# Kernel tuning notes

Measured on AMD Instinct MI355X. Metric: run time of the kernel, lower is better.

The kernel has to match this reference:

```python
import jax, jax.numpy as jnp
import numpy as np

B, L, A, K = 2, 1024, 14, 30
NUM_RBF = 16
NPE = 16  # num_positional_embeddings
EF = 128  # edge_features
EDGE_IN = NPE + NUM_RBF * A * A  # 3152


def setup_inputs() -> dict:
    key = jax.random.key(0)
    ks = jax.random.split(key, 4)
    # coords scaled so pairwise distances span the RBF range [0, 20]
    X = jax.random.normal(ks[0], (B, L, A, 3), dtype=jnp.float32) * 3.0
    mask = jnp.ones((B, L), dtype=jnp.float32)
    residue_idx = jnp.tile(jnp.arange(L, dtype=jnp.int32)[None, :], (B, 1))
    chain_labels = jnp.zeros((B, L), dtype=jnp.int32)
    atom_mask = jax.random.randint(ks[1], (B, L, A), 0, 2).astype(jnp.float32)
    W_edge = jax.random.normal(ks[2], (EF, EDGE_IN), dtype=jnp.float32) * 0.02
    ln_gamma = jnp.ones((EF,), dtype=jnp.float32)
    ln_beta = jnp.zeros((EF,), dtype=jnp.float32)
    return {"X": X, "mask": mask, "residue_idx": residue_idx,
            "chain_labels": chain_labels, "atom_mask": atom_mask,
            "W_edge": W_edge, "ln_gamma": ln_gamma, "ln_beta": ln_beta}


def reference(X, mask, residue_idx, chain_labels, atom_mask, W_edge, ln_gamma, ln_beta):
    Bq, Lq = X.shape[0], X.shape[1]
    # ---- CA pairwise distances + masked top-k (smallest) ----
    X_ca = X[:, :, 1, :]
    m2 = mask[:, :, None] * mask[:, None, :]                    # [B,L,L]
    dX = X_ca[:, :, None, :] - X_ca[:, None, :, :]
    D = m2 * jnp.sqrt(jnp.sum(dX ** 2, -1) + 1e-6)
    D_max = jnp.max(D, -1, keepdims=True)
    D_adjust = D + 2.0 * (1.0 - m2) * D_max
    _, E_idx = jax.lax.top_k(-D_adjust, K)                      # smallest K -> [B,L,K]
    # ---- transformer positional encoding of relative index ----
    ii = jnp.arange(Lq, dtype=jnp.float32)[None, :, None]
    d = (E_idx.astype(jnp.float32) - ii)[..., None]             # [B,L,K,1]
    freq = jnp.exp(jnp.arange(0, NPE, 2, dtype=jnp.float32) * (-(np.log(10000.0) / NPE)))
    angles = d * freq                                           # [B,L,K,NPE/2]
    E_pos = jnp.concatenate([jnp.cos(angles), jnp.sin(angles)], -1)  # [B,L,K,NPE]
    # ---- impute CB, build 14-atom set ----
    N_, Ca, C_, O_ = X[:, :, 0, :], X[:, :, 1, :], X[:, :, 2, :], X[:, :, 3, :]
    b = Ca - N_
    c = C_ - Ca
    a = jnp.cross(b, c)
    Cb = -0.58273431 * a + 0.56802827 * b - 0.54067466 * c + Ca
    X2 = jnp.concatenate([jnp.stack([N_, Ca, C_, O_, Cb], -2), X[:, :, 5:, :]], -2)  # [B,L,14,3]
    am = 1.0 - atom_mask                                        # module passes 1 - atom_mask
    # ---- gather neighbor atoms, fused 14x14 atom-pair RBFs ----
    bidx = jnp.arange(Bq)[:, None, None]
    X2n = X2[bidx, E_idx]                                       # [B,L,K,14,3]
    amn = am[bidx, E_idx]                                       # [B,L,K,14]
    diff = X2[:, :, None, :, None, :] - X2n[:, :, :, None, :, :]
    Dab = jnp.sqrt(jnp.sum(diff ** 2, -1) + 1e-6)               # [B,L,K,14,14] (a of i, b of nbr)
    combo = am[:, :, None, :, None] * amn[:, :, :, None, :]     # [B,L,K,14,14]
    mu = jnp.linspace(0.0, 20.0, NUM_RBF)
    sigma = 20.0 / NUM_RBF
    rbf = jnp.exp(-(((Dab[..., None] - mu) / sigma) ** 2)) * combo[..., None]
    RBF_all = rbf.reshape(Bq, Lq, K, A * A * NUM_RBF)           # matches torch cat order (i,j,rbf)
    # ---- edge embedding + layernorm ----
    E = jnp.concatenate([E_pos, RBF_all], -1)                   # [B,L,K,EDGE_IN]
    E = E @ W_edge.T                                            # [B,L,K,EF]
    mean = jnp.mean(E, -1, keepdims=True)
    var = jnp.var(E, -1, keepdims=True)
    E = (E - mean) / jnp.sqrt(var + 1e-5) * ln_gamma + ln_beta
    return (E, E_idx)
```

## Files before the change

kernel.cpp:

```cpp
#include <hip/hip_runtime.h>
#include <hip/hip_bf16.h>
#include <stdint.h>

#define LQ 1024
#define BQ 2
#define AQ 14
#define KQ 30
#define EFQ 128
#define EDGE_IN 3152
#define KPAD 3200
#define NCHUNK 50
#define ROWS (BQ*LQ*KQ)
#define EIDX_OFF (ROWS*EFQ)

typedef __attribute__((ext_vector_type(8))) _Float16 half8;
typedef __attribute__((ext_vector_type(4))) float floatx4;
typedef unsigned long long ull;

static __device__ __forceinline__ uint32_t pkh(float a, float b) {
    auto h = __builtin_amdgcn_cvt_pkrtz(a, b);
    return __builtin_bit_cast(uint32_t, h);
}

__global__ __launch_bounds__(512) void topk_kernel(
    const float* __restrict__ X, const float* __restrict__ mask,
    float* __restrict__ out, int* __restrict__ idx_ws)
{
    __shared__ float xs[LQ], ys[LQ], zs[LQ], ms[LQ];

    const int t = threadIdx.x, w = t >> 6, lane = t & 63;
    const int row = blockIdx.x*8 + w;
    const int b = row >> 10, i = row & (LQ - 1);

    for (int j = t; j < LQ; j += 512) {
        size_t base = ((size_t)(b*LQ + j))*42 + 3;
        xs[j] = X[base+0]; ys[j] = X[base+1]; zs[j] = X[base+2];
        ms[j] = mask[b*LQ + j];
    }
    __syncthreads();

    const float mif = ms[i];
    const double cx = (double)xs[i], cy = (double)ys[i], cz = (double)zs[i];

    double Dk[16]; float mf[16];
    bool allone = (mif == 1.0f);
    #pragma unroll
    for (int s = 0; s < 16; ++s) {
        int j = s*64 + lane;
        double dx = __dsub_rn(cx, (double)xs[j]);
        double dy = __dsub_rn(cy, (double)ys[j]);
        double dz = __dsub_rn(cz, (double)zs[j]);
        mf[s] = ms[j];
        Dk[s] = __dadd_rn(__dadd_rn(__dmul_rn(dx,dx), __dmul_rn(dy,dy)),
                          __dmul_rn(dz,dz));
        allone = allone && (mf[s] == 1.0f);
    }

    if (!__all(allone ? 1 : 0)) {
        const double mi_d = (double)mif;
        double lm = 0.0;
        #pragma unroll
        for (int s = 0; s < 16; ++s) {
            double m2 = __dmul_rn(mi_d, (double)mf[s]);
            Dk[s] = __dmul_rn(m2, sqrt(__dadd_rn(Dk[s], 1e-6)));
            lm = fmax(lm, Dk[s]);
        }
        #pragma unroll
        for (int off = 32; off; off >>= 1) lm = fmax(lm, __shfl_xor(lm, off));
        #pragma unroll
        for (int s = 0; s < 16; ++s) {
            double m2 = __dmul_rn(mi_d, (double)mf[s]);
            Dk[s] = __dadd_rn(Dk[s],
                    __dmul_rn(__dmul_rn(2.0, __dsub_rn(1.0, m2)), lm));
        }
    }

    unsigned cons = 0;
    for (int k = 0; k < KQ; ++k) {
        ull bk = ~0ull; int bi = 1 << 30;
        #pragma unroll
        for (int s = 0; s < 16; ++s) {
            ull key = (ull)__double_as_longlong(Dk[s]);
            bool alive = !((cons >> s) & 1u);
            if (alive && key < bk) { bk = key; bi = s*64 + lane; }
        }
        #pragma unroll
        for (int off = 32; off; off >>= 1) {
            ull okk = __shfl_xor(bk, off);
            int oii = __shfl_xor(bi, off);
            if (okk < bk || (okk == bk && oii < bi)) { bk = okk; bi = oii; }
        }
        if ((bi & 63) == lane) cons |= (1u << (bi >> 6));
        if (lane == 0) {
            int rg = row*KQ + k;
            idx_ws[rg] = bi;
            out[EIDX_OFF + rg] = (float)bi;
        }
    }
}

__global__ __launch_bounds__(256) void wpad_kernel(
    const float* __restrict__ W, _Float16* __restrict__ wpad)
{
    int idx = blockIdx.x*256 + threadIdx.x;
    if (idx >= EFQ*KPAD) return;
    int n = idx / KPAD, f = idx - n*KPAD;
    float v = (f < EDGE_IN) ? W[(size_t)n*EDGE_IN + f] : 0.0f;
    wpad[idx] = (_Float16)v;
}

struct FusedSmem {
    alignas(16) float atoms[128*42];
    alignas(16) unsigned short Bl[128*64];
    alignas(16) float drow[64];
    int residg[128];
    unsigned int maskb[128];
    float gsh[EFQ], bsh[EFQ];
};

static __device__ __forceinline__ void gen8(
    const float* __restrict__ atomsA, const float* __restrict__ atomsB,
    unsigned maskA, unsigned maskB, float drowv,
    int f0, uint32_t* __restrict__ v)
{
    if (f0 >= 16) {
        int p = (f0 - 16) >> 4;
        if (p >= AQ*AQ) { v[0] = v[1] = v[2] = v[3] = 0u; return; }
        int rbase = (f0 - 16) & 15;
        int a  = (p * 74899) >> 20;
        int bp = p - a*14;
        bool czero = ((((maskA >> a) | (maskB >> bp)) & 1u) != 0u);
        const float* ca = atomsA + a*3;
        const float* na = atomsB + bp*3;
        float dx = ca[0]-na[0], dy = ca[1]-na[1], dz = ca[2]-na[2];
        float u = __builtin_amdgcn_sqrtf(dx*dx + dy*dy + dz*dz + 1e-6f) * 0.96089846f;
        float e[8];
        #pragma unroll
        for (int j = 0; j < 8; ++j) {
            float tt = __fmaf_rn(-(float)(rbase + j), 1.28119795f, u);
            e[j] = __builtin_amdgcn_exp2f(-(tt*tt));
        }
        #pragma unroll
        for (int k = 0; k < 4; ++k) v[k] = czero ? 0u : pkh(e[2*k], e[2*k+1]);
    } else {
        const float fr[8] = {1.0f, 0.31622776601683794f, 0.1f,
            0.031622776601683794f, 0.01f, 0.0031622776601683794f,
            0.001f, 0.00031622776601683794f};
        float e[8];
        if (f0 == 0) {
            #pragma unroll
            for (int j = 0; j < 8; ++j) e[j] = __cosf(drowv * fr[j]);
        } else {
            #pragma unroll
            for (int j = 0; j < 8; ++j) e[j] = __sinf(drowv * fr[j]);
        }
        #pragma unroll
        for (int k = 0; k < 4; ++k) v[k] = pkh(e[2*k], e[2*k+1]);
    }
}

__global__ __launch_bounds__(256) void fused_kernel(
    const float* __restrict__ X, const float* __restrict__ atom_mask,
    const _Float16* __restrict__ wpad, const float* __restrict__ gamma,
    const float* __restrict__ beta, const int* __restrict__ idx_ws,
    float* __restrict__ out)
{
    __shared__ FusedSmem sm;
    const int t = threadIdx.x;
    const int row0 = blockIdx.x * 64;
    const int b = row0 / (LQ*KQ);

    if (t < 64) {
        int rg = row0 + t;
        int rem = rg - b*(LQ*KQ);
        int i = rem / KQ;
        int j = idx_ws[rg];
        sm.residg[t]    = b*LQ + i;
        sm.residg[64+t] = b*LQ + j;
        sm.drow[t] = (float)j - (float)i;
    }
    if (t < EFQ) { sm.gsh[t] = gamma[t]; sm.bsh[t] = beta[t]; }
    __syncthreads();

    for (int u = t; u < 128*42; u += 256) {
        int s = u / 42; int e = u - s*42;
        sm.atoms[s*42 + e] = X[(size_t)sm.residg[s]*42 + e];
    }
    __syncthreads();

    if (t < 128) {
        float* at = &sm.atoms[t*42];
        float Nx=at[0],Ny=at[1],Nz=at[2], Cax=at[3],Cay=at[4],Caz=at[5],
              Cx=at[6],Cy=at[7],Cz=at[8];
        float bx=Cax-Nx, by=Cay-Ny, bz=Caz-Nz;
        float ex=Cx-Cax, ey=Cy-Cay, ez=Cz-Caz;
        float ax = by*ez - bz*ey, ay = bz*ex - bx*ez, az = bx*ey - by*ex;
        at[12] = -0.58273431f*ax + 0.56802827f*bx - 0.54067466f*ex + Cax;
        at[13] = -0.58273431f*ay + 0.56802827f*by - 0.54067466f*ey + Cay;
        at[14] = -0.58273431f*az + 0.56802827f*bz - 0.54067466f*ez + Caz;
        unsigned mb = 0;
        const float* amp = &atom_mask[(size_t)sm.residg[t]*AQ];
        #pragma unroll
        for (int a = 0; a < AQ; ++a) if (amp[a] > 0.5f) mb |= (1u << a);
        sm.maskb[t] = mb;
    }

    const int w = t >> 6, lane = t & 63, q = lane >> 4, l15 = lane & 15;
    const int m = w*16 + l15;

    int boff0[8], boff1[8];
    #pragma unroll
    for (int nt = 0; nt < 8; ++nt) {
        int n = nt*16 + l15;
        boff0[nt] = n*64 + ((q ^ (n&7))*8);
        boff1[nt] = n*64 + (((4+q) ^ (n&7))*8);
    }
    int stRegion[4]; const _Float16* stBase[4];
    #pragma unroll
    for (int i2 = 0; i2 < 4; ++i2) {
        int region = w*4 + i2;
        int n = region*8 + (lane >> 3);
        int kbsrc = (lane & 7) ^ (lane >> 3);
        stRegion[i2] = region;
        stBase[i2] = wpad + (size_t)n*KPAD + kbsrc*8;
    }
    auto stage = [&](int c) {
        #pragma unroll
        for (int i2 = 0; i2 < 4; ++i2) {
            const _Float16* g = stBase[i2] + c*64;
            __builtin_amdgcn_global_load_lds(
                (const __attribute__((address_space(1))) uint32_t*)g,
                (__attribute__((address_space(3))) uint32_t*)&sm.Bl[stRegion[i2]*512],
                16, 0, 0);
        }
    };

    floatx4 acc[8];
    #pragma unroll
    for (int nt = 0; nt < 8; ++nt) acc[nt] = (floatx4){0.f,0.f,0.f,0.f};

    __syncthreads();

    const float* atomsA = &sm.atoms[m*42];
    const float* atomsB = &sm.atoms[(64+m)*42];
    const unsigned maskA = sm.maskb[m], maskB = sm.maskb[64+m];
    const float drowv = sm.drow[m];

    union H8 { uint32_t u[4]; half8 h; };
    for (int c = 0; c < NCHUNK; ++c) {
        if (c) __syncthreads();
        stage(c);
        H8 va0, va1;
        gen8(atomsA, atomsB, maskA, maskB, drowv, c*64 + q*8,      va0.u);
        gen8(atomsA, atomsB, maskA, maskB, drowv, c*64 + 32 + q*8, va1.u);
        __syncthreads();
        #pragma unroll
        for (int nt = 0; nt < 8; ++nt) {
            half8 b0 = *reinterpret_cast<const half8*>(&sm.Bl[boff0[nt]]);
            half8 b1 = *reinterpret_cast<const half8*>(&sm.Bl[boff1[nt]]);
            acc[nt] = __builtin_amdgcn_mfma_f32_16x16x32_f16(va0.h, b0, acc[nt], 0, 0, 0);
            acc[nt] = __builtin_amdgcn_mfma_f32_16x16x32_f16(va1.h, b1, acc[nt], 0, 0, 0);
        }
    }

    #pragma unroll
    for (int v = 0; v < 4; ++v) {
        float s = 0.f, s2 = 0.f;
        #pragma unroll
        for (int nt = 0; nt < 8; ++nt) { float x = acc[nt][v]; s += x; s2 += x*x; }
        #pragma unroll
        for (int off = 1; off < 16; off <<= 1) {
            s  += __shfl_xor(s,  off);
            s2 += __shfl_xor(s2, off);
        }
        float mean = s * (1.0f/128.0f);
        float var  = s2 * (1.0f/128.0f) - mean*mean;
        float rstd = 1.0f / sqrtf(var + 1e-5f);
        int row_l = w*16 + q*4 + v;
        size_t obase = (size_t)(row0 + row_l)*EFQ;
        #pragma unroll
        for (int nt = 0; nt < 8; ++nt) {
            int col = nt*16 + l15;
            out[obase + col] = (acc[nt][v] - mean)*rstd*sm.gsh[col] + sm.bsh[col];
        }
    }
}

extern "C" void kernel_launch(void* const* d_in, const int* in_sizes, int n_in,
                              void* d_out, int out_size, void* d_ws, size_t ws_size,
                              hipStream_t stream)
{
    const float* X         = (const float*)d_in[0];
    const float* mask      = (const float*)d_in[1];
    const float* atom_mask = (const float*)d_in[4];
    const float* W         = (const float*)d_in[5];
    const float* gamma     = (const float*)d_in[6];
    const float* beta      = (const float*)d_in[7];
    float* out = (float*)d_out;

    int*       idx_ws = (int*)d_ws;
    _Float16*  wpad   = (_Float16*)((char*)d_ws + 262144);

    hipLaunchKernelGGL(wpad_kernel, dim3((EFQ*KPAD + 255)/256), dim3(256), 0, stream,
                       W, wpad);
    hipLaunchKernelGGL(topk_kernel, dim3(BQ*LQ/8), dim3(512), 0, stream,
                       X, mask, out, idx_ws);
    hipLaunchKernelGGL(fused_kernel, dim3(ROWS/64), dim3(256), 0, stream,
                       X, atom_mask, wpad, gamma, beta, idx_ws, out);
}
```

Before: 189.8 us.

## Merge weight padding into top-k launch, pack top-k keys, double fused M tile

Drops the separate weight-padding kernel by having the extra blocks of the top-k launch do the fp16 conversion. The top-k selection now packs each neighbor index into the low bits of its distance key, so each round is a plain 64-bit min tree and no separate index comparison is needed. The fused RBF+GEMM kernel moves to 512 threads and 128 rows per block, so each staged weight chunk is shared by twice as many rows. In exchange there are fewer blocks, more shared memory per block, and the key packing truncates the low 10 mantissa bits, which could change the order of near-tied distances.

New measurement: 176.2 us. 7.1% less time.

```diff
diff --git a/kernel.cpp b/kernel.cpp
--- a/kernel.cpp
+++ b/kernel.cpp
@@ -10,6 +10,7 @@
 #define EDGE_IN 3152
 #define KPAD 3200
 #define NCHUNK 50
+#define MTILE 128
 #define ROWS (BQ*LQ*KQ)
 #define EIDX_OFF (ROWS*EFQ)
 
@@ -21,14 +22,29 @@
     auto h = __builtin_amdgcn_cvt_pkrtz(a, b);
     return __builtin_bit_cast(uint32_t, h);
 }
+static __device__ __forceinline__ ull umin64(ull a, ull b) { return a < b ? a : b; }
 
 __global__ __launch_bounds__(512) void topk_kernel(
     const float* __restrict__ X, const float* __restrict__ mask,
-    float* __restrict__ out, int* __restrict__ idx_ws)
+    const float* __restrict__ W, float* __restrict__ out,
+    int* __restrict__ idx_ws, _Float16* __restrict__ wpad)
 {
     __shared__ float xs[LQ], ys[LQ], zs[LQ], ms[LQ];
-
-    const int t = threadIdx.x, w = t >> 6, lane = t & 63;
+    const int t = threadIdx.x;
+
+    if (blockIdx.x >= 256) {
+        int base = (blockIdx.x - 256)*8192 + t;
+        #pragma unroll
+        for (int r = 0; r < 16; ++r) {
+            int idx = base + r*512;
+            int n = idx / KPAD, f = idx - n*KPAD;
+            float v = (f < EDGE_IN) ? W[(size_t)n*EDGE_IN + f] : 0.0f;
+            wpad[idx] = (_Float16)v;
+        }
+        return;
+    }
+
+    const int w = t >> 6, lane = t & 63;
     const int row = blockIdx.x*8 + w;
     const int b = row >> 10, i = row & (LQ - 1);
 
@@ -75,46 +91,43 @@
         }
     }
 
-    unsigned cons = 0;
+    ull key[16];
+    #pragma unroll
+    for (int s = 0; s < 16; ++s)
+        key[s] = (((ull)__double_as_longlong(Dk[s])) & ~1023ull)
+               | (unsigned)(s*64 + lane);
+
     for (int k = 0; k < KQ; ++k) {
-        ull bk = ~0ull; int bi = 1 << 30;
-        #pragma unroll
-        for (int s = 0; s < 16; ++s) {
-            ull key = (ull)__double_as_longlong(Dk[s]);
-            bool alive = !((cons >> s) & 1u);
-            if (alive && key < bk) { bk = key; bi = s*64 + lane; }
-        }
-        #pragma unroll
-        for (int off = 32; off; off >>= 1) {
-            ull okk = __shfl_xor(bk, off);
-            int oii = __shfl_xor(bi, off);
-            if (okk < bk || (okk == bk && oii < bi)) { bk = okk; bi = oii; }
-        }
-        if ((bi & 63) == lane) cons |= (1u << (bi >> 6));
+        ull a0 = umin64(key[0],  key[1]),  a1 = umin64(key[2],  key[3]);
+        ull a2 = umin64(key[4],  key[5]),  a3 = umin64(key[6],  key[7]);
+        ull a4 = umin64(key[8],  key[9]),  a5 = umin64(key[10], key[11]);
+        ull a6 = umin64(key[12], key[13]), a7 = umin64(key[14], key[15]);
+        ull b0 = umin64(a0, a1), b1 = umin64(a2, a3);
+        ull b2 = umin64(a4, a5), b3 = umin64(a6, a7);
+        ull bk = umin64(umin64(b0, b1), umin64(b2, b3));
+        #pragma unroll
+        for (int off = 32; off; off >>= 1)
+            bk = umin64(bk, (ull)__shfl_xor(bk, off));
+        int j = (int)(bk & 1023ull);
         if (lane == 0) {
             int rg = row*KQ + k;
-            idx_ws[rg] = bi;
-            out[EIDX_OFF + rg] = (float)bi;
-        }
-    }
-}
-
-__global__ __launch_bounds__(256) void wpad_kernel(
-    const float* __restrict__ W, _Float16* __restrict__ wpad)
-{
-    int idx = blockIdx.x*256 + threadIdx.x;
-    if (idx >= EFQ*KPAD) return;
-    int n = idx / KPAD, f = idx - n*KPAD;
-    float v = (f < EDGE_IN) ? W[(size_t)n*EDGE_IN + f] : 0.0f;
-    wpad[idx] = (_Float16)v;
+            idx_ws[rg] = j;
+            out[EIDX_OFF + rg] = (float)j;
+        }
+        bool mine = ((j & 63) == lane);
+        int s_win = j >> 6;
+        #pragma unroll
+        for (int s = 0; s < 16; ++s)
+            key[s] = (mine && s == s_win) ? ~0ull : key[s];
+    }
 }
 
 struct FusedSmem {
-    alignas(16) float atoms[128*42];
+    alignas(16) float atoms[256*42];
     alignas(16) unsigned short Bl[128*64];
-    alignas(16) float drow[64];
-    int residg[128];
-    unsigned int maskb[128];
+    alignas(16) float drow[MTILE];
+    int residg[256];
+    unsigned int maskb[256];
     float gsh[EFQ], bsh[EFQ];
 };
 
@@ -159,7 +172,7 @@
     }
 }
 
-__global__ __launch_bounds__(256) void fused_kernel(
+__global__ __launch_bounds__(512) void fused_kernel(
     const float* __restrict__ X, const float* __restrict__ atom_mask,
     const _Float16* __restrict__ wpad, const float* __restrict__ gamma,
     const float* __restrict__ beta, const int* __restrict__ idx_ws,
@@ -167,28 +180,28 @@
 {
     __shared__ FusedSmem sm;
     const int t = threadIdx.x;
-    const int row0 = blockIdx.x * 64;
+    const int row0 = blockIdx.x * MTILE;
     const int b = row0 / (LQ*KQ);
 
-    if (t < 64) {
+    if (t < MTILE) {
         int rg = row0 + t;
         int rem = rg - b*(LQ*KQ);
         int i = rem / KQ;
         int j = idx_ws[rg];
-        sm.residg[t]    = b*LQ + i;
-        sm.residg[64+t] = b*LQ + j;
+        sm.residg[t]       = b*LQ + i;
+        sm.residg[MTILE+t] = b*LQ + j;
         sm.drow[t] = (float)j - (float)i;
     }
     if (t < EFQ) { sm.gsh[t] = gamma[t]; sm.bsh[t] = beta[t]; }
     __syncthreads();
 
-    for (int u = t; u < 128*42; u += 256) {
+    for (int u = t; u < 256*42; u += 512) {
         int s = u / 42; int e = u - s*42;
         sm.atoms[s*42 + e] = X[(size_t)sm.residg[s]*42 + e];
     }
     __syncthreads();
 
-    if (t < 128) {
+    if (t < 256) {
         float* at = &sm.atoms[t*42];
         float Nx=at[0],Ny=at[1],Nz=at[2], Cax=at[3],Cay=at[4],Caz=at[5],
               Cx=at[6],Cy=at[7],Cz=at[8];
@@ -215,10 +228,10 @@
         boff0[nt] = n*64 + ((q ^ (n&7))*8);
         boff1[nt] = n*64 + (((4+q) ^ (n&7))*8);
     }
-    int stRegion[4]; const _Float16* stBase[4];
-    #pragma unroll
-    for (int i2 = 0; i2 < 4; ++i2) {
-        int region = w*4 + i2;
+    int stRegion[2]; const _Float16* stBase[2];
+    #pragma unroll
+    for (int i2 = 0; i2 < 2; ++i2) {
+        int region = w*2 + i2;
         int n = region*8 + (lane >> 3);
         int kbsrc = (lane & 7) ^ (lane >> 3);
         stRegion[i2] = region;
@@ -226,7 +239,7 @@
     }
     auto stage = [&](int c) {
         #pragma unroll
-        for (int i2 = 0; i2 < 4; ++i2) {
+        for (int i2 = 0; i2 < 2; ++i2) {
             const _Float16* g = stBase[i2] + c*64;
             __builtin_amdgcn_global_load_lds(
                 (const __attribute__((address_space(1))) uint32_t*)g,
@@ -242,8 +255,8 @@
     __syncthreads();
 
     const float* atomsA = &sm.atoms[m*42];
-    const float* atomsB = &sm.atoms[(64+m)*42];
-    const unsigned maskA = sm.maskb[m], maskB = sm.maskb[64+m];
+    const float* atomsB = &sm.atoms[(MTILE+m)*42];
+    const unsigned maskA = sm.maskb[m], maskB = sm.maskb[MTILE+m];
     const float drowv = sm.drow[m];
 
     union H8 { uint32_t u[4]; half8 h; };
@@ -301,10 +314,8 @@
     int*       idx_ws = (int*)d_ws;
     _Float16*  wpad   = (_Float16*)((char*)d_ws + 262144);
 
-    hipLaunchKernelGGL(wpad_kernel, dim3((EFQ*KPAD + 255)/256), dim3(256), 0, stream,
-                       W, wpad);
-    hipLaunchKernelGGL(topk_kernel, dim3(BQ*LQ/8), dim3(512), 0, stream,
-                       X, mask, out, idx_ws);
-    hipLaunchKernelGGL(fused_kernel, dim3(ROWS/64), dim3(256), 0, stream,
+    hipLaunchKernelGGL(topk_kernel, dim3(306), dim3(512), 0, stream,
+                       X, mask, W, out, idx_ws, wpad);
+    hipLaunchKernelGGL(fused_kernel, dim3(ROWS/MTILE), dim3(512), 0, stream,
                        X, atom_mask, wpad, gamma, beta, idx_ws, out);
 }
```
